# Kernel tuning notes

Hardware: AMD Instinct MI355X
Metric: run time of the kernel (lower is better)

The kernel has to match this reference:

```python
import jax, jax.numpy as jnp
import numpy as np

H = 4  # heads


def _tconv(x, src, dst, ea, Wq, bq, Wk, bk, Wv, bv, We, Ws, bs):
    # PyG TransformerConv, heads=4, concat=False, root_weight=True, beta=False
    N = x.shape[0]
    Dh = Wq.shape[1] // H  # per-head dim (= hidden_channels)
    q = (x @ Wq + bq).reshape(N, H, Dh)
    k = (x @ Wk + bk).reshape(N, H, Dh)
    v = (x @ Wv + bv).reshape(N, H, Dh)
    e = (ea @ We).reshape(-1, H, Dh)      # lin_edge has no bias in PyG
    kj = k[src] + e                        # [E, H, Dh]
    vj = v[src] + e                        # [E, H, Dh]
    alpha = (q[dst] * kj).sum(-1) / jnp.sqrt(jnp.asarray(Dh, x.dtype))  # [E, H]
    # segment softmax over incoming edges of each dst node
    m = jax.ops.segment_max(alpha, dst, num_segments=N)
    a = jnp.exp(alpha - m[dst])
    s = jax.ops.segment_sum(a, dst, num_segments=N)
    a = a / (s[dst] + 1e-16)
    out = jax.ops.segment_sum(a[:, :, None] * vj, dst, num_segments=N)  # [N, H, Dh]
    out = out.mean(axis=1)                 # concat=False -> mean over heads
    return out + x @ Ws + bs               # root/skip connection


def setup_inputs() -> dict:
    key = jax.random.key(0)
    ks = jax.random.split(key, 32)
    N, E, C_in, C_e, Ch = 50000, 800000, 32, 16, 32
    d = {}
    d['x'] = jax.random.normal(ks[0], (N, C_in), dtype=jnp.float32)
    d['edge_attr'] = jax.random.normal(ks[1], (E, C_e), dtype=jnp.float32)
    d['edge_index'] = jax.random.randint(ks[2], (2, E), 0, N, dtype=jnp.int32)
    s = 0.05
    i = 3
    for L, cin in ((1, C_in), (2, Ch)):
        d[f'Wq{L}'] = jax.random.normal(ks[i], (cin, H * Ch)) * s; i += 1
        d[f'bq{L}'] = jnp.zeros((H * Ch,), jnp.float32)
        d[f'Wk{L}'] = jax.random.normal(ks[i], (cin, H * Ch)) * s; i += 1
        d[f'bk{L}'] = jnp.zeros((H * Ch,), jnp.float32)
        d[f'Wv{L}'] = jax.random.normal(ks[i], (cin, H * Ch)) * s; i += 1
        d[f'bv{L}'] = jnp.zeros((H * Ch,), jnp.float32)
        d[f'We{L}'] = jax.random.normal(ks[i], (C_e, H * Ch)) * s; i += 1
        d[f'Ws{L}'] = jax.random.normal(ks[i], (cin, Ch)) * s; i += 1
        d[f'bs{L}'] = jnp.zeros((Ch,), jnp.float32)
    d['Wm1'] = jax.random.normal(ks[i], (2 * Ch + C_e, Ch)) * s; i += 1
    d['bm1'] = jnp.zeros((Ch,), jnp.float32)
    d['Wm2'] = jax.random.normal(ks[i], (Ch, 1)) * s; i += 1
    d['bm2'] = jnp.zeros((1,), jnp.float32)
    return d


def reference(x, edge_attr, edge_index,
              Wq1, bq1, Wk1, bk1, Wv1, bv1, We1, Ws1, bs1,
              Wq2, bq2, Wk2, bk2, Wv2, bv2, We2, Ws2, bs2,
              Wm1, bm1, Wm2, bm2):
    src, dst = edge_index[0], edge_index[1]
    h = jax.nn.relu(_tconv(x, src, dst, edge_attr, Wq1, bq1, Wk1, bk1, Wv1, bv1, We1, Ws1, bs1))
    h = jax.nn.relu(_tconv(h, src, dst, edge_attr, Wq2, bq2, Wk2, bk2, Wv2, bv2, We2, Ws2, bs2))
    ef = jnp.concatenate([h[src], edge_attr, h[dst]], axis=-1)  # [E, 2*Ch + C_e]
    out = jax.nn.relu(ef @ Wm1 + bm1) @ Wm2 + bm2
    return out.reshape(-1)
```

## Files before the change

kernel.cpp:

```cpp
#include <hip/hip_runtime.h>
#include <hip/hip_fp16.h>
#include <math.h>

#define D128 128
#define CH32 32
#define CE16 16

__global__ void k_hist(const int* __restrict__ dst, int* __restrict__ deg, int E) {
    int e = blockIdx.x * blockDim.x + threadIdx.x;
    if (e < E) atomicAdd(&deg[dst[e]], 1);
}

__global__ void k_scan1(const int* __restrict__ deg, int* __restrict__ offs,
                        int* __restrict__ bsum, int N) {
    __shared__ int buf[256];
    int t = threadIdx.x;
    int i = blockIdx.x * 256 + t;
    int v = (i < N) ? deg[i] : 0;
    buf[t] = v;
    __syncthreads();
    #pragma unroll
    for (int off = 1; off < 256; off <<= 1) {
        int val = (t >= off) ? buf[t - off] : 0;
        __syncthreads();
        buf[t] += val;
        __syncthreads();
    }
    if (i < N) offs[i] = buf[t] - v;
    if (t == 255) bsum[blockIdx.x] = buf[255];
}

__global__ void k_scan2(const int* __restrict__ bsum, int* __restrict__ boff, int nb) {
    __shared__ int buf[256];
    int t = threadIdx.x;
    int v = (t < nb) ? bsum[t] : 0;
    buf[t] = v;
    __syncthreads();
    #pragma unroll
    for (int off = 1; off < 256; off <<= 1) {
        int val = (t >= off) ? buf[t - off] : 0;
        __syncthreads();
        buf[t] += val;
        __syncthreads();
    }
    if (t < nb) boff[t] = buf[t] - v;
}

__global__ void k_scan3(const int* __restrict__ boff, int* __restrict__ offs,
                        int* __restrict__ cur, int N, int E) {
    int i = blockIdx.x * blockDim.x + threadIdx.x;
    if (i < N) {
        int o = offs[i] + boff[i >> 8];
        offs[i] = o;
        cur[i] = o;
    }
    if (i == 0) offs[N] = E;
}

__global__ void k_scatter(const int* __restrict__ src, const int* __restrict__ dst,
                          int* __restrict__ cur, int* __restrict__ csr_srcb,
                          float4* __restrict__ ea_csr4, const float4* __restrict__ ea4,
                          int E) {
    int e = blockIdx.x * blockDim.x + threadIdx.x;
    if (e < E) {
        int d = dst[e];
        int p = atomicAdd(&cur[d], 1);
        csr_srcb[p] = src[e] << 9;
        float4 a0 = ea4[e * 4 + 0];
        float4 a1 = ea4[e * 4 + 1];
        float4 a2 = ea4[e * 4 + 2];
        float4 a3 = ea4[e * 4 + 3];
        ea_csr4[p * 4 + 0] = a0;
        ea_csr4[p * 4 + 1] = a1;
        ea_csr4[p * 4 + 2] = a2;
        ea_csr4[p * 4 + 3] = a3;
    }
}

__global__ __launch_bounds__(128) void k_nodeproj(
    const float* __restrict__ xin,
    const float* __restrict__ Wq, const float* __restrict__ bq,
    const float* __restrict__ Wk, const float* __restrict__ bk,
    const float* __restrict__ Wv, const float* __restrict__ bv,
    const float* __restrict__ Ws, const float* __restrict__ bs,
    float* __restrict__ q, __half* __restrict__ kvh,
    float* __restrict__ skip, int N)
{
    int tid = threadIdx.x;
    int c   = tid & 31;
    int pos = ((tid >> 1) << 2) | (tid & 1);
    float wq[32], wk[32], wv[32], ws[32];
    #pragma unroll
    for (int j = 0; j < 32; j++) {
        wq[j] = Wq[j * D128 + tid];
        wk[j] = Wk[j * D128 + tid];
        wv[j] = Wv[j * D128 + tid];
        ws[j] = Ws[j * CH32 + c];
    }
    float bqc = bq[tid], bkc = bk[tid], bvc = bv[tid], bsc = bs[c];
    __shared__ float xs[4][32];
    int nchunk = (N + 3) / 4;
    for (int chk = blockIdx.x; chk < nchunk; chk += gridDim.x) {
        int base = chk * 4;
        {
            int r = tid >> 5;
            int n = base + r;
            xs[r][c] = (n < N) ? xin[n * 32 + c] : 0.f;
        }
        __syncthreads();
        #pragma unroll
        for (int r = 0; r < 4; r++) {
            int n = base + r;
            if (n < N) {
                float aq = bqc, ak = bkc, av = bvc;
                #pragma unroll
                for (int j = 0; j < 32; j++) {
                    float xj = xs[r][j];
                    aq = fmaf(xj, wq[j], aq);
                    ak = fmaf(xj, wk[j], ak);
                    av = fmaf(xj, wv[j], av);
                }
                q[n * D128 + tid] = aq;
                kvh[(size_t)n * 256 + pos]     = __float2half_rn(ak);
                kvh[(size_t)n * 256 + pos + 2] = __float2half_rn(av);
            }
        }
        {
            int r = tid >> 5;
            int n = base + r;
            if (n < N) {
                float as = bsc;
                #pragma unroll
                for (int j = 0; j < 32; j++) as = fmaf(xs[r][j], ws[j], as);
                skip[n * 32 + c] = as;
            }
        }
        __syncthreads();
    }
}

__global__ __launch_bounds__(64) void k_edgeattn(
    const float* __restrict__ q, const __half* __restrict__ kvh,
    const float* __restrict__ skip,
    const float* __restrict__ ea_csr, const float* __restrict__ We,
    const int* __restrict__ offs, const int* __restrict__ csr_srcb,
    float* __restrict__ hout)
{
    int node = blockIdx.x;
    int lane = threadIdx.x;
    int col2 = lane << 1;
    int lan15 = lane & 15;

    float2 we[16];
    #pragma unroll
    for (int j = 0; j < 16; j++)
        we[j] = *(const float2*)&We[j * D128 + col2];

    const float QS = 0.17677669529663687f * 1.4426950408889634f;
    float2 qv = *(const float2*)&q[(size_t)node * D128 + col2];
    qv.x *= QS; qv.y *= QS;

    float qe = 0.f;
    #pragma unroll
    for (int j = 0; j < 16; j++) {
        float t = fmaf(qv.y, we[j].y, qv.x * we[j].x);
        t += __shfl_xor(t, 1);
        t += __shfl_xor(t, 2);
        t += __shfl_xor(t, 4);
        t += __shfl_xor(t, 8);
        if (lan15 == j) qe = t;
    }

    int s0 = offs[node], s1 = offs[node + 1];
    int deg = s1 - s0;

    float l = 0.f, ac0 = 0.f, ac1 = 0.f, sea = 0.f;

    if (deg > 0) {
        int last = s1 - 1;
        const char* kvb = (const char*)kvh;
        int toff8 = lane << 3;

        auto ldidx = [&](int e) { return csr_srcb[min(e, last)]; };
        auto ldkv  = [&](int ib) {
            return *(const float2*)(kvb + (size_t)(unsigned)ib + toff8);
        };
        auto ldea  = [&](int e) {
            return ea_csr[(size_t)min(e, last) * 16 + lan15];
        };
        auto edge = [&](const float2& raw, float eav, bool valid) {
            float2 kf = __half22float2(*(const __half2*)&raw.x);
            float2 vf = __half22float2(*(const __half2*)&raw.y);
            float t = fmaf(qv.x, kf.x, fmaf(qv.y, kf.y, qe * eav));
            t += __shfl_xor(t, 1);
            t += __shfl_xor(t, 2);
            t += __shfl_xor(t, 4);
            t += __shfl_xor(t, 8);
            float p = valid ? __builtin_amdgcn_exp2f(t) : 0.f;
            l += p;
            ac0 = fmaf(p, vf.x, ac0);
            ac1 = fmaf(p, vf.y, ac1);
            sea = fmaf(p, eav, sea);
        };

        int iA0 = ldidx(s0 + 0), iA1 = ldidx(s0 + 1);
        int iA2 = ldidx(s0 + 2), iA3 = ldidx(s0 + 3);
        int iB0 = ldidx(s0 + 4), iB1 = ldidx(s0 + 5);
        int iB2 = ldidx(s0 + 6), iB3 = ldidx(s0 + 7);
        float2 kA0 = ldkv(iA0), kA1 = ldkv(iA1), kA2 = ldkv(iA2), kA3 = ldkv(iA3);
        float  eA0 = ldea(s0 + 0), eA1 = ldea(s0 + 1);
        float  eA2 = ldea(s0 + 2), eA3 = ldea(s0 + 3);

        int base = s0;
        int nIter = (deg + 7) >> 3;
        for (int it = 0; it < nIter; ++it) {
            float2 kB0 = ldkv(iB0), kB1 = ldkv(iB1);
            float2 kB2 = ldkv(iB2), kB3 = ldkv(iB3);
            float  eB0 = ldea(base + 4), eB1 = ldea(base + 5);
            float  eB2 = ldea(base + 6), eB3 = ldea(base + 7);
            iA0 = ldidx(base + 8);  iA1 = ldidx(base + 9);
            iA2 = ldidx(base + 10); iA3 = ldidx(base + 11);

            edge(kA0, eA0, base + 0 <= last);
            edge(kA1, eA1, base + 1 <= last);
            edge(kA2, eA2, base + 2 <= last);
            edge(kA3, eA3, base + 3 <= last);

            kA0 = ldkv(iA0); kA1 = ldkv(iA1); kA2 = ldkv(iA2); kA3 = ldkv(iA3);
            eA0 = ldea(base + 8);  eA1 = ldea(base + 9);
            eA2 = ldea(base + 10); eA3 = ldea(base + 11);
            iB0 = ldidx(base + 12); iB1 = ldidx(base + 13);
            iB2 = ldidx(base + 14); iB3 = ldidx(base + 15);

            edge(kB0, eB0, base + 4 <= last);
            edge(kB1, eB1, base + 5 <= last);
            edge(kB2, eB2, base + 6 <= last);
            edge(kB3, eB3, base + 7 <= last);

            base += 8;
        }
    }

    float inv = 1.0f / (l + 1e-16f);
    float se = sea * inv;
    float r0 = ac0 * inv;
    float r1 = ac1 * inv;
    int gbase = lane & 48;
    #pragma unroll
    for (int j = 0; j < 16; j++) {
        float sj = __shfl(se, gbase | j, 64);
        r0 = fmaf(sj, we[j].x, r0);
        r1 = fmaf(sj, we[j].y, r1);
    }
    r0 += __shfl_xor(r0, 16);   r1 += __shfl_xor(r1, 16);
    r0 += __shfl_xor(r0, 32);   r1 += __shfl_xor(r1, 32);
    if (lane < 16) {
        const float2 sk = *(const float2*)&skip[(size_t)node * 32 + col2];
        float o0 = fmaxf(fmaf(0.25f, r0, sk.x), 0.f);
        float o1 = fmaxf(fmaf(0.25f, r1, sk.y), 0.f);
        *(float2*)&hout[(size_t)node * 32 + col2] = make_float2(o0, o1);
    }
}

__global__ __launch_bounds__(256) void k_mlp(
    const float* __restrict__ h, const float* __restrict__ ea,
    const int* __restrict__ src, const int* __restrict__ dst,
    const float* __restrict__ Wm1, const float* __restrict__ bm1,
    const float* __restrict__ Wm2, const float* __restrict__ bm2,
    float* __restrict__ out, int E)
{
    __shared__ float4 W4[80 * 8];
    __shared__ float bm1L[32];
    __shared__ float wm2L[32];
    int tid = threadIdx.x;
    const float4* Wm1_4 = (const float4*)Wm1;
    for (int i = tid; i < 640; i += 256) W4[i] = Wm1_4[i];
    if (tid < 32) { bm1L[tid] = bm1[tid]; wm2L[tid] = Wm2[tid]; }
    __syncthreads();

    int e = blockIdx.x * 256 + tid;
    if (e >= E) return;
    float b2 = bm2[0];
    int s = src[e], d = dst[e];

    float4 acc[8];
    #pragma unroll
    for (int i = 0; i < 8; i++) acc[i] = make_float4(0.f, 0.f, 0.f, 0.f);

    auto dorow = [&](int j, float xj) {
        #pragma unroll
        for (int c4 = 0; c4 < 8; c4++) {
            float4 w = W4[j * 8 + c4];
            acc[c4].x = fmaf(xj, w.x, acc[c4].x);
            acc[c4].y = fmaf(xj, w.y, acc[c4].y);
            acc[c4].z = fmaf(xj, w.z, acc[c4].z);
            acc[c4].w = fmaf(xj, w.w, acc[c4].w);
        }
    };

    const float4* hs  = (const float4*)(h + (size_t)s * 32);
    const float4* hd  = (const float4*)(h + (size_t)d * 32);
    const float4* eav = (const float4*)(ea + (size_t)e * 16);
    #pragma unroll
    for (int qd = 0; qd < 8; qd++) {
        float4 xv = hs[qd];
        dorow(qd * 4 + 0, xv.x); dorow(qd * 4 + 1, xv.y);
        dorow(qd * 4 + 2, xv.z); dorow(qd * 4 + 3, xv.w);
    }
    #pragma unroll
    for (int qd = 0; qd < 4; qd++) {
        float4 xv = eav[qd];
        dorow(32 + qd * 4 + 0, xv.x); dorow(32 + qd * 4 + 1, xv.y);
        dorow(32 + qd * 4 + 2, xv.z); dorow(32 + qd * 4 + 3, xv.w);
    }
    #pragma unroll
    for (int qd = 0; qd < 8; qd++) {
        float4 xv = hd[qd];
        dorow(48 + qd * 4 + 0, xv.x); dorow(48 + qd * 4 + 1, xv.y);
        dorow(48 + qd * 4 + 2, xv.z); dorow(48 + qd * 4 + 3, xv.w);
    }

    float y = b2;
    #pragma unroll
    for (int c4 = 0; c4 < 8; c4++) {
        y += fmaxf(acc[c4].x + bm1L[c4 * 4 + 0], 0.f) * wm2L[c4 * 4 + 0];
        y += fmaxf(acc[c4].y + bm1L[c4 * 4 + 1], 0.f) * wm2L[c4 * 4 + 1];
        y += fmaxf(acc[c4].z + bm1L[c4 * 4 + 2], 0.f) * wm2L[c4 * 4 + 2];
        y += fmaxf(acc[c4].w + bm1L[c4 * 4 + 3], 0.f) * wm2L[c4 * 4 + 3];
    }
    out[e] = y;
}

extern "C" void kernel_launch(void* const* d_in, const int* in_sizes, int n_in,
                              void* d_out, int out_size, void* d_ws, size_t ws_size,
                              hipStream_t stream)
{
    const float* x  = (const float*)d_in[0];
    const float* ea = (const float*)d_in[1];
    const int*   ei = (const int*)d_in[2];
    const int N = in_sizes[0] / 32;
    const int E = in_sizes[1] / 16;
    const int* src = ei;
    const int* dst = ei + E;

    const float *Wq1 = (const float*)d_in[3],  *bq1 = (const float*)d_in[4];
    const float *Wk1 = (const float*)d_in[5],  *bk1 = (const float*)d_in[6];
    const float *Wv1 = (const float*)d_in[7],  *bv1 = (const float*)d_in[8];
    const float *We1 = (const float*)d_in[9],  *Ws1 = (const float*)d_in[10];
    const float *bs1 = (const float*)d_in[11];
    const float *Wq2 = (const float*)d_in[12], *bq2 = (const float*)d_in[13];
    const float *Wk2 = (const float*)d_in[14], *bk2 = (const float*)d_in[15];
    const float *Wv2 = (const float*)d_in[16], *bv2 = (const float*)d_in[17];
    const float *We2 = (const float*)d_in[18], *Ws2 = (const float*)d_in[19];
    const float *bs2 = (const float*)d_in[20];
    const float *Wm1 = (const float*)d_in[21], *bm1 = (const float*)d_in[22];
    const float *Wm2 = (const float*)d_in[23], *bm2 = (const float*)d_in[24];

    char* w = (char*)d_ws;
    auto alloc = [&](size_t bytes) -> void* {
        void* p = (void*)w;
        w += (bytes + 255) & ~(size_t)255;
        return p;
    };
    int* deg      = (int*)alloc((size_t)N * 4);
    int* offs     = (int*)alloc(((size_t)N + 1) * 4);
    int* cur      = (int*)alloc((size_t)N * 4);
    int* bsum     = (int*)alloc(256 * 4);
    int* boff     = (int*)alloc(256 * 4);
    int* csr_srcb = (int*)alloc((size_t)E * 4);
    float* ea_csr = (float*)alloc((size_t)E * 16 * 4);
    float* qb     = (float*)alloc((size_t)N * 128 * 4);
    __half* kvb   = (__half*)alloc((size_t)N * 256 * 2);
    float* skipb  = (float*)alloc((size_t)N * 32 * 4);
    float* h1     = (float*)alloc((size_t)N * 32 * 4);
    float* h2     = (float*)alloc((size_t)N * 32 * 4);

    hipMemsetAsync(deg, 0, (size_t)N * 4, stream);

    int ebl = (E + 255) / 256;
    int nb  = (N + 255) / 256;
    k_hist<<<ebl, 256, 0, stream>>>(dst, deg, E);
    k_scan1<<<nb, 256, 0, stream>>>(deg, offs, bsum, N);
    k_scan2<<<1, 256, 0, stream>>>(bsum, boff, nb);
    k_scan3<<<nb, 256, 0, stream>>>(boff, offs, cur, N, E);
    k_scatter<<<ebl, 256, 0, stream>>>(src, dst, cur, csr_srcb,
                                       (float4*)ea_csr, (const float4*)ea, E);

    k_nodeproj<<<1024, 128, 0, stream>>>(x, Wq1, bq1, Wk1, bk1, Wv1, bv1, Ws1, bs1,
                                         qb, kvb, skipb, N);
    k_edgeattn<<<N, 64, 0, stream>>>(qb, kvb, skipb, ea_csr, We1,
                                     offs, csr_srcb, h1);
    k_nodeproj<<<1024, 128, 0, stream>>>(h1, Wq2, bq2, Wk2, bk2, Wv2, bv2, Ws2, bs2,
                                         qb, kvb, skipb, N);
    k_edgeattn<<<N, 64, 0, stream>>>(qb, kvb, skipb, ea_csr, We2,
                                     offs, csr_srcb, h2);
    k_mlp<<<ebl, 256, 0, stream>>>(h2, ea, src, dst, Wm1, bm1, Wm2, bm2,
                                   (float*)d_out, E);
}
```

Baseline: 546.8 us.

## Process two edges per wavefront in edge attention with 4-column lanes

Splits the 64-lane wavefront into two 32-lane halves that each handle a different incoming edge, with every lane owning 4 of the 128 columns. The K/V half-precision layout is changed so each lane fetches 16 bytes per edge. Partial softmax sums are merged across the halves at the end. This halves the shuffle-reduction work per edge and widens gather loads, but uses more registers for accumulators and reloads We from global memory in the epilogue instead of keeping it in registers.

After: 542.9 us. Within noise of the previous version (-0.7%).

```diff
diff --git a/kernel.cpp b/kernel.cpp
--- a/kernel.cpp
+++ b/kernel.cpp
@@ -88,7 +88,7 @@
 {
     int tid = threadIdx.x;
     int c   = tid & 31;
-    int pos = ((tid >> 1) << 2) | (tid & 1);
+    int pos = ((tid >> 2) << 3) | (tid & 3);
     float wq[32], wk[32], wv[32], ws[32];
     #pragma unroll
     for (int j = 0; j < 32; j++) {
@@ -122,7 +122,7 @@
                 }
                 q[n * D128 + tid] = aq;
                 kvh[(size_t)n * 256 + pos]     = __float2half_rn(ak);
-                kvh[(size_t)n * 256 + pos + 2] = __float2half_rn(av);
+                kvh[(size_t)n * 256 + pos + 4] = __float2half_rn(av);
             }
         }
         {
@@ -148,117 +148,132 @@
 {
     int node = blockIdx.x;
     int lane = threadIdx.x;
-    int col2 = lane << 1;
-    int lan15 = lane & 15;
-
-    float2 we[16];
-    #pragma unroll
-    for (int j = 0; j < 16; j++)
-        we[j] = *(const float2*)&We[j * D128 + col2];
+    int eg   = lane >> 5;
+    int c    = lane & 31;
+    int g    = c & 7;
+    int c4   = c << 2;
 
     const float QS = 0.17677669529663687f * 1.4426950408889634f;
-    float2 qv = *(const float2*)&q[(size_t)node * D128 + col2];
-    qv.x *= QS; qv.y *= QS;
-
-    float qe = 0.f;
+    float4 qv = *(const float4*)&q[(size_t)node * D128 + c4];
+    qv.x *= QS; qv.y *= QS; qv.z *= QS; qv.w *= QS;
+
+    float qe0 = 0.f, qe1 = 0.f;
     #pragma unroll
     for (int j = 0; j < 16; j++) {
-        float t = fmaf(qv.y, we[j].y, qv.x * we[j].x);
+        float4 wj = *(const float4*)&We[j * D128 + c4];
+        float t = fmaf(qv.w, wj.w, fmaf(qv.z, wj.z, fmaf(qv.y, wj.y, qv.x * wj.x)));
         t += __shfl_xor(t, 1);
         t += __shfl_xor(t, 2);
         t += __shfl_xor(t, 4);
-        t += __shfl_xor(t, 8);
-        if (lan15 == j) qe = t;
+        if (g == (j >> 1)) { if (j & 1) qe1 = t; else qe0 = t; }
     }
 
     int s0 = offs[node], s1 = offs[node + 1];
     int deg = s1 - s0;
 
-    float l = 0.f, ac0 = 0.f, ac1 = 0.f, sea = 0.f;
+    float l = 0.f;
+    float ac0 = 0.f, ac1 = 0.f, ac2 = 0.f, ac3 = 0.f;
+    float se0 = 0.f, se1 = 0.f;
 
     if (deg > 0) {
         int last = s1 - 1;
         const char* kvb = (const char*)kvh;
-        int toff8 = lane << 3;
-
-        auto ldidx = [&](int e) { return csr_srcb[min(e, last)]; };
+        int toff = c << 4;
+
+        auto eidx = [&](int p) { return min(s0 + 2 * p + eg, last); };
+        auto ldidx = [&](int p) { return csr_srcb[eidx(p)]; };
         auto ldkv  = [&](int ib) {
-            return *(const float2*)(kvb + (size_t)(unsigned)ib + toff8);
+            return *(const float4*)(kvb + (size_t)(unsigned)ib + toff);
         };
-        auto ldea  = [&](int e) {
-            return ea_csr[(size_t)min(e, last) * 16 + lan15];
+        auto ldea  = [&](int p) {
+            return *(const float2*)&ea_csr[(size_t)eidx(p) * 16 + 2 * g];
         };
-        auto edge = [&](const float2& raw, float eav, bool valid) {
-            float2 kf = __half22float2(*(const __half2*)&raw.x);
-            float2 vf = __half22float2(*(const __half2*)&raw.y);
-            float t = fmaf(qv.x, kf.x, fmaf(qv.y, kf.y, qe * eav));
+        auto pair = [&](const float4& kvr, const float2& eav, int p) {
+            bool valid = (s0 + 2 * p + eg) <= last;
+            float2 k01 = __half22float2(*(const __half2*)&kvr.x);
+            float2 k23 = __half22float2(*(const __half2*)&kvr.y);
+            float2 v01 = __half22float2(*(const __half2*)&kvr.z);
+            float2 v23 = __half22float2(*(const __half2*)&kvr.w);
+            float t = fmaf(qv.y, k01.y, qv.x * k01.x);
+            t = fmaf(qv.z, k23.x, t);
+            t = fmaf(qv.w, k23.y, t);
+            t = fmaf(qe0, eav.x, t);
+            t = fmaf(qe1, eav.y, t);
             t += __shfl_xor(t, 1);
             t += __shfl_xor(t, 2);
             t += __shfl_xor(t, 4);
-            t += __shfl_xor(t, 8);
-            float p = valid ? __builtin_amdgcn_exp2f(t) : 0.f;
-            l += p;
-            ac0 = fmaf(p, vf.x, ac0);
-            ac1 = fmaf(p, vf.y, ac1);
-            sea = fmaf(p, eav, sea);
+            float pp = valid ? __builtin_amdgcn_exp2f(t) : 0.f;
+            l += pp;
+            ac0 = fmaf(pp, v01.x, ac0);
+            ac1 = fmaf(pp, v01.y, ac1);
+            ac2 = fmaf(pp, v23.x, ac2);
+            ac3 = fmaf(pp, v23.y, ac3);
+            se0 = fmaf(pp, eav.x, se0);
+            se1 = fmaf(pp, eav.y, se1);
         };
 
-        int iA0 = ldidx(s0 + 0), iA1 = ldidx(s0 + 1);
-        int iA2 = ldidx(s0 + 2), iA3 = ldidx(s0 + 3);
-        int iB0 = ldidx(s0 + 4), iB1 = ldidx(s0 + 5);
-        int iB2 = ldidx(s0 + 6), iB3 = ldidx(s0 + 7);
-        float2 kA0 = ldkv(iA0), kA1 = ldkv(iA1), kA2 = ldkv(iA2), kA3 = ldkv(iA3);
-        float  eA0 = ldea(s0 + 0), eA1 = ldea(s0 + 1);
-        float  eA2 = ldea(s0 + 2), eA3 = ldea(s0 + 3);
-
-        int base = s0;
+        int iA0 = ldidx(0), iA1 = ldidx(1);
+        int iB0 = ldidx(2), iB1 = ldidx(3);
+        float4 kA0 = ldkv(iA0), kA1 = ldkv(iA1);
+        float2 eA0 = ldea(0),   eA1 = ldea(1);
+
+        int p = 0;
         int nIter = (deg + 7) >> 3;
         for (int it = 0; it < nIter; ++it) {
-            float2 kB0 = ldkv(iB0), kB1 = ldkv(iB1);
-            float2 kB2 = ldkv(iB2), kB3 = ldkv(iB3);
-            float  eB0 = ldea(base + 4), eB1 = ldea(base + 5);
-            float  eB2 = ldea(base + 6), eB3 = ldea(base + 7);
-            iA0 = ldidx(base + 8);  iA1 = ldidx(base + 9);
-            iA2 = ldidx(base + 10); iA3 = ldidx(base + 11);
-
-            edge(kA0, eA0, base + 0 <= last);
-            edge(kA1, eA1, base + 1 <= last);
-            edge(kA2, eA2, base + 2 <= last);
-            edge(kA3, eA3, base + 3 <= last);
-
-            kA0 = ldkv(iA0); kA1 = ldkv(iA1); kA2 = ldkv(iA2); kA3 = ldkv(iA3);
-            eA0 = ldea(base + 8);  eA1 = ldea(base + 9);
-            eA2 = ldea(base + 10); eA3 = ldea(base + 11);
-            iB0 = ldidx(base + 12); iB1 = ldidx(base + 13);
-            iB2 = ldidx(base + 14); iB3 = ldidx(base + 15);
-
-            edge(kB0, eB0, base + 4 <= last);
-            edge(kB1, eB1, base + 5 <= last);
-            edge(kB2, eB2, base + 6 <= last);
-            edge(kB3, eB3, base + 7 <= last);
-
-            base += 8;
+            float4 kB0 = ldkv(iB0), kB1 = ldkv(iB1);
+            float2 eB0 = ldea(p + 2), eB1 = ldea(p + 3);
+            iA0 = ldidx(p + 4); iA1 = ldidx(p + 5);
+
+            pair(kA0, eA0, p + 0);
+            pair(kA1, eA1, p + 1);
+
+            kA0 = ldkv(iA0); kA1 = ldkv(iA1);
+            eA0 = ldea(p + 4); eA1 = ldea(p + 5);
+            iB0 = ldidx(p + 6); iB1 = ldidx(p + 7);
+
+            pair(kB0, eB0, p + 2);
+            pair(kB1, eB1, p + 3);
+
+            p += 4;
         }
     }
 
+    asm volatile("" ::: "memory");
+
+    l   += __shfl_xor(l, 32);
+    ac0 += __shfl_xor(ac0, 32);
+    ac1 += __shfl_xor(ac1, 32);
+    ac2 += __shfl_xor(ac2, 32);
+    ac3 += __shfl_xor(ac3, 32);
+    se0 += __shfl_xor(se0, 32);
+    se1 += __shfl_xor(se1, 32);
+
     float inv = 1.0f / (l + 1e-16f);
-    float se = sea * inv;
-    float r0 = ac0 * inv;
-    float r1 = ac1 * inv;
-    int gbase = lane & 48;
+    float r0 = ac0 * inv, r1 = ac1 * inv, r2 = ac2 * inv, r3 = ac3 * inv;
+    float sn0 = se0 * inv, sn1 = se1 * inv;
+
+    int gb = lane & ~7;
     #pragma unroll
     for (int j = 0; j < 16; j++) {
-        float sj = __shfl(se, gbase | j, 64);
-        r0 = fmaf(sj, we[j].x, r0);
-        r1 = fmaf(sj, we[j].y, r1);
-    }
-    r0 += __shfl_xor(r0, 16);   r1 += __shfl_xor(r1, 16);
-    r0 += __shfl_xor(r0, 32);   r1 += __shfl_xor(r1, 32);
-    if (lane < 16) {
-        const float2 sk = *(const float2*)&skip[(size_t)node * 32 + col2];
-        float o0 = fmaxf(fmaf(0.25f, r0, sk.x), 0.f);
-        float o1 = fmaxf(fmaf(0.25f, r1, sk.y), 0.f);
-        *(float2*)&hout[(size_t)node * 32 + col2] = make_float2(o0, o1);
+        float sj = __shfl((j & 1) ? sn1 : sn0, gb | (j >> 1), 64);
+        float4 wj = *(const float4*)&We[j * D128 + c4];
+        r0 = fmaf(sj, wj.x, r0);
+        r1 = fmaf(sj, wj.y, r1);
+        r2 = fmaf(sj, wj.z, r2);
+        r3 = fmaf(sj, wj.w, r3);
+    }
+    r0 += __shfl_xor(r0, 8);  r0 += __shfl_xor(r0, 16);
+    r1 += __shfl_xor(r1, 8);  r1 += __shfl_xor(r1, 16);
+    r2 += __shfl_xor(r2, 8);  r2 += __shfl_xor(r2, 16);
+    r3 += __shfl_xor(r3, 8);  r3 += __shfl_xor(r3, 16);
+    if (lane < 8) {
+        const float4 sk = *(const float4*)&skip[(size_t)node * 32 + c4];
+        float4 o;
+        o.x = fmaxf(fmaf(0.25f, r0, sk.x), 0.f);
+        o.y = fmaxf(fmaf(0.25f, r1, sk.y), 0.f);
+        o.z = fmaxf(fmaf(0.25f, r2, sk.z), 0.f);
+        o.w = fmaxf(fmaf(0.25f, r3, sk.w), 0.f);
+        *(float4*)&hout[(size_t)node * 32 + c4] = o;
     }
 }
 
```
